# Performance work log

Measured on AMD Instinct MI355X. Metric: run time of the kernel, lower is better.

## Reference

```python
import jax, jax.numpy as jnp
import numpy as np

N, E, DIN, DH, ED, H, C = 50000, 800000, 384, 256, 32, 4, 64
EPS = 1e-5


def setup_inputs() -> dict:
    key = jax.random.key(0)
    ks = jax.random.split(key, 32)
    w = lambda k, shape, fan: (jax.random.normal(k, shape, jnp.float32) / np.float32(np.sqrt(fan)))
    inp = {
        'x': jax.random.normal(ks[0], (N, DIN), jnp.float32),
        'edge_index': jax.random.randint(ks[1], (2, E), 0, N, dtype=jnp.int32),
        'edge_attr': jax.random.normal(ks[2], (E, ED), jnp.float32),
        'W_in': w(ks[3], (DIN, DH), DIN), 'b_in': jnp.zeros((DH,), jnp.float32),
        'W_out': w(ks[4], (DH, DH), DH), 'b_out': jnp.zeros((DH,), jnp.float32),
    }
    for i in range(2):
        o = 5 + 6 * i
        inp[f'Wl{i}'] = w(ks[o + 0], (DH, H * C), DH)
        inp[f'bl{i}'] = jnp.zeros((H * C,), jnp.float32)
        inp[f'Wr{i}'] = w(ks[o + 1], (DH, H * C), DH)
        inp[f'br{i}'] = jnp.zeros((H * C,), jnp.float32)
        inp[f'We{i}'] = w(ks[o + 2], (ED, H * C), ED)
        inp[f'att{i}'] = w(ks[o + 3], (H, C), C)
        inp[f'bias{i}'] = jnp.zeros((H * C,), jnp.float32)
        inp[f'g{i}'] = jnp.ones((DH,), jnp.float32)
        inp[f'beta{i}'] = jnp.zeros((DH,), jnp.float32)
    return inp


def _gatv2(h, src, dst, ea, Wl, bl, Wr, br, We, att, bias):
    # h: [N, DH]; src/dst: [Etot]; ea: [Etot, ED]
    xl = (h @ Wl + bl).reshape(N, H, C)
    xr = (h @ Wr + br).reshape(N, H, C)
    ee = (ea @ We).reshape(-1, H, C)
    m = jax.nn.leaky_relu(xl[src] + xr[dst] + ee, 0.2)  # [Etot,H,C]
    logits = jnp.einsum('ehc,hc->eh', m, att)           # [Etot,H]
    mx = jax.ops.segment_max(logits, dst, num_segments=N)
    p = jnp.exp(logits - mx[dst])
    den = jax.ops.segment_sum(p, dst, num_segments=N)
    alpha = p / den[dst]                                # softmax per dst node
    out = jax.ops.segment_sum(xl[src] * alpha[:, :, None], dst, num_segments=N)
    return out.reshape(N, H * C) + bias


def _graph_norm(h, g, beta):
    # PyG LayerNorm(mode='graph'), batch=None: normalize over all nodes & channels
    mu = h.mean()
    hc = h - mu
    var = (hc * hc).mean()
    return hc / jnp.sqrt(var + EPS) * g + beta


def reference(x, edge_index, edge_attr, W_in, b_in,
              Wl0, bl0, Wr0, br0, We0, att0, bias0, g0, beta0,
              Wl1, bl1, Wr1, br1, We1, att1, bias1, g1, beta1,
              W_out, b_out):
    loops = jnp.arange(N, dtype=edge_index.dtype)
    src = jnp.concatenate([edge_index[0], loops])
    dst = jnp.concatenate([edge_index[1], loops])
    # self-loop edge_attr filled with mean edge feature (PyG fill_value='mean')
    ea = jnp.concatenate([edge_attr, jnp.broadcast_to(edge_attr.mean(0), (N, ED))], axis=0)
    h = jax.nn.relu(x @ W_in + b_in)
    layers = ((Wl0, bl0, Wr0, br0, We0, att0, bias0, g0, beta0),
              (Wl1, bl1, Wr1, br1, We1, att1, bias1, g1, beta1))
    for Wl, bl, Wr, br, We, att, bias, g, beta in layers:
        hn = jax.nn.elu(_gatv2(h, src, dst, ea, Wl, bl, Wr, br, We, att, bias))
        h = _graph_norm(h + hn, g, beta)
    return h @ W_out + b_out
```

## Files before the change

### kernel.cpp

```cpp
#include <hip/hip_runtime.h>
#include <hip/hip_bf16.h>

#define N_NODES 50000
#define E_EDGES 800000
#define DIN_K   384
#define DH_N    256
#define EPSN    1e-5f

typedef unsigned short ushortT;
typedef __attribute__((ext_vector_type(4))) float f32x4;
typedef __attribute__((ext_vector_type(8))) short bf16x8;

static __device__ __forceinline__ float bf2f(unsigned short u)
{
    return __uint_as_float(((unsigned)u) << 16);
}
static __device__ __forceinline__ unsigned short f2bf(float f)
{
    unsigned u = __float_as_uint(f);
    unsigned r = (u + 0x7fffu + ((u >> 16) & 1u)) >> 16;
    return (unsigned short)r;
}
static __device__ __forceinline__ unsigned pack2(float a, float b)
{
    return (unsigned)f2bf(a) | ((unsigned)f2bf(b) << 16);
}

__global__ __launch_bounds__(256) void ea_accum_kernel(const float* __restrict__ ea,
                                                       float* __restrict__ accum, long total)
{
    long stride = (long)gridDim.x * blockDim.x;
    float local = 0.f;
    for (long i = (long)blockIdx.x * blockDim.x + threadIdx.x; i < total; i += stride)
        local += ea[i];
    __shared__ float red[256];
    red[threadIdx.x] = local;
    __syncthreads();
    if (threadIdx.x < 32) {
        float s = 0.f;
#pragma unroll
        for (int r = 0; r < 8; ++r) s += red[r * 32 + threadIdx.x];
        atomicAdd(&accum[threadIdx.x], s);
    }
}

__global__ void hist_kernel(const int* __restrict__ dst, int* __restrict__ counts, int E)
{
    int stride = gridDim.x * blockDim.x;
    for (int e = blockIdx.x * blockDim.x + threadIdx.x; e < E; e += stride)
        atomicAdd(&counts[dst[e]], 1);
}

__global__ __launch_bounds__(1024) void scan_kernel(const int* __restrict__ counts,
                                                    int* __restrict__ offsets, int Nn)
{
    __shared__ int sdata[1024];
    __shared__ int run_s;
    int tid = threadIdx.x;
    if (tid == 0) run_s = 0;
    __syncthreads();
    for (int base2 = 0; base2 < Nn; base2 += 1024) {
        int i = base2 + tid;
        int v = (i < Nn) ? counts[i] : 0;
        sdata[tid] = v;
        __syncthreads();
        for (int off = 1; off < 1024; off <<= 1) {
            int t = (tid >= off) ? sdata[tid - off] : 0;
            __syncthreads();
            sdata[tid] += t;
            __syncthreads();
        }
        int run = run_s;
        if (i < Nn) offsets[i] = run + sdata[tid] - v;
        int tot = sdata[1023];
        __syncthreads();
        if (tid == 0) run_s = run + tot;
        __syncthreads();
    }
    if (tid == 0) offsets[Nn] = run_s;
}

__global__ void scatter_kernel(const int* __restrict__ src, const int* __restrict__ dst,
                               const int* __restrict__ offsets, int* __restrict__ cursors,
                               int* __restrict__ s_src, int* __restrict__ s_dst,
                               int* __restrict__ s_eid, int E)
{
    int stride = gridDim.x * blockDim.x;
    for (int e = blockIdx.x * blockDim.x + threadIdx.x; e < E; e += stride) {
        int d = dst[e];
        int p = offsets[d] + atomicAdd(&cursors[d], 1);
        s_src[p] = src[e];
        s_dst[p] = d;
        s_eid[p] = e;
    }
}

__global__ void eemean_kernel(const float* __restrict__ accum,
                              const float* __restrict__ We0, const float* __restrict__ We1,
                              float* __restrict__ eemean, float invE)
{
    int tid = threadIdx.x;
    int layer = tid >> 8, c = tid & 255;
    const float* W = layer ? We1 : We0;
    float s = 0.f;
#pragma unroll
    for (int j = 0; j < 32; ++j) s += accum[j] * invE * W[j * 256 + c];
    eemean[layer * 256 + c] = s;
}

__global__ __launch_bounds__(256) void transpose_bf16_kernel(const float* __restrict__ in,
                                                             ushortT* __restrict__ out,
                                                             int K, int N)
{
    __shared__ float tile[32][33];
    int bx = blockIdx.x * 32;
    int by = blockIdx.y * 32;
    int tx = threadIdx.x & 31, ty = threadIdx.x >> 5;
#pragma unroll
    for (int r = 0; r < 32; r += 8) {
        int k = by + ty + r, n = bx + tx;
        if (k < K && n < N) tile[ty + r][tx] = in[(size_t)k * N + n];
    }
    __syncthreads();
#pragma unroll
    for (int r = 0; r < 32; r += 8) {
        int n = bx + ty + r, k = by + tx;
        if (n < N && k < K) out[(size_t)n * K + k] = f2bf(tile[tx][ty + r]);
    }
}

__global__ void fuse_bias_kernel(const float* __restrict__ bl, const float* __restrict__ br,
                                 float* __restrict__ out)
{
    int i = threadIdx.x;
    out[i] = (i < 256) ? bl[i] : br[i - 256];
}

__global__ __launch_bounds__(256) void mfma_gemm_kernel(
    const float* __restrict__ A, const ushortT* __restrict__ Bt,
    const float* __restrict__ bias, float* __restrict__ Cf,
    ushortT* __restrict__ Cb, int K, int Nn, int act)
{
    __shared__ __align__(16) ushortT As[128 * 32];
    __shared__ __align__(16) ushortT Bs[128 * 32];
    int tid = threadIdx.x;
    int brow = blockIdx.x * 128;
    int bcol = blockIdx.y * 128;
    int lane = tid & 63, w = tid >> 6;
    int wr = w >> 1, wc = w & 1;
    int fr = lane & 15, fq = lane >> 4;

    f32x4 acc[4][4];
#pragma unroll
    for (int i = 0; i < 4; ++i)
#pragma unroll
        for (int j = 0; j < 4; ++j)
            acc[i][j] = (f32x4){0.f, 0.f, 0.f, 0.f};

    int r0 = tid >> 2, g0 = tid & 3;
    int r1 = r0 + 64;
    int arow0 = brow + r0, arow1 = brow + r1;
    bool av0 = arow0 < N_NODES, av1 = arow1 < N_NODES;
    const float* Ap0 = A + (size_t)arow0 * K + g0 * 8;
    const float* Ap1 = A + (size_t)arow1 * K + g0 * 8;
    const ushortT* Bp0 = Bt + (size_t)(bcol + r0) * K + g0 * 8;
    const ushortT* Bp1 = Bt + (size_t)(bcol + r1) * K + g0 * 8;
    uint4* asw0 = (uint4*)&As[(size_t)tid * 8];
    uint4* asw1 = (uint4*)&As[(size_t)(tid + 256) * 8];
    uint4* bsw0 = (uint4*)&Bs[(size_t)tid * 8];
    uint4* bsw1 = (uint4*)&Bs[(size_t)(tid + 256) * 8];

    for (int k0 = 0; k0 < K; k0 += 32) {
        float4 z = make_float4(0.f, 0.f, 0.f, 0.f);
        float4 fa0 = z, fa1 = z, fc0 = z, fc1 = z;
        if (av0) { fa0 = *(const float4*)(Ap0 + k0); fc0 = *(const float4*)(Ap0 + k0 + 4); }
        if (av1) { fa1 = *(const float4*)(Ap1 + k0); fc1 = *(const float4*)(Ap1 + k0 + 4); }
        uint4 ub0 = *(const uint4*)(Bp0 + k0);
        uint4 ub1 = *(const uint4*)(Bp1 + k0);
        uint4 ua0, ua1;
        ua0.x = pack2(fa0.x, fa0.y); ua0.y = pack2(fa0.z, fa0.w);
        ua0.z = pack2(fc0.x, fc0.y); ua0.w = pack2(fc0.z, fc0.w);
        ua1.x = pack2(fa1.x, fa1.y); ua1.y = pack2(fa1.z, fa1.w);
        ua1.z = pack2(fc1.x, fc1.y); ua1.w = pack2(fc1.z, fc1.w);
        __syncthreads();
        *asw0 = ua0; *asw1 = ua1;
        *bsw0 = ub0; *bsw1 = ub1;
        __syncthreads();

        bf16x8 af[4], bfv[4];
#pragma unroll
        for (int mi = 0; mi < 4; ++mi)
            af[mi] = *(bf16x8*)&As[(size_t)(wr * 64 + mi * 16 + fr) * 32 + fq * 8];
#pragma unroll
        for (int ni = 0; ni < 4; ++ni)
            bfv[ni] = *(bf16x8*)&Bs[(size_t)(wc * 64 + ni * 16 + fr) * 32 + fq * 8];
#pragma unroll
        for (int mi = 0; mi < 4; ++mi)
#pragma unroll
            for (int ni = 0; ni < 4; ++ni)
                acc[mi][ni] = __builtin_amdgcn_mfma_f32_16x16x32_bf16(
                    af[mi], bfv[ni], acc[mi][ni], 0, 0, 0);
    }

#pragma unroll
    for (int ni = 0; ni < 4; ++ni) {
        int col = bcol + wc * 64 + ni * 16 + fr;
        float bv = bias[col];
#pragma unroll
        for (int mi = 0; mi < 4; ++mi) {
#pragma unroll
            for (int r = 0; r < 4; ++r) {
                int row = brow + wr * 64 + mi * 16 + fq * 4 + r;
                if (row < N_NODES) {
                    float t = acc[mi][ni][r] + bv;
                    if (act == 1) t = t > 0.f ? t : 0.f;
                    if (Cf) Cf[(size_t)row * Nn + col] = t;
                    if (Cb) Cb[(size_t)row * Nn + col] = f2bf(t);
                }
            }
        }
    }
}

__global__ __launch_bounds__(256) void edge_logits_kernel(
    const float* __restrict__ ea, const int* __restrict__ s_eid,
    const int* __restrict__ s_src, const int* __restrict__ s_dst,
    const float* __restrict__ We, const float* __restrict__ att,
    const ushortT* __restrict__ xlr, float* __restrict__ logits)
{
    __shared__ float As[32][68];
    __shared__ float Bs[32][256];
    __shared__ int   sidx[64], didx[64];
    int tid = threadIdx.x;
    int brow = blockIdx.x * 64;

#pragma unroll
    for (int t = 0; t < 8; ++t) {
        int f4 = tid + t * 256;
        int kr = f4 >> 6, cq = f4 & 63;
        *(float4*)&Bs[kr][(cq & 3) * 64 + (cq >> 2) * 4] =
            *(const float4*)(We + (size_t)kr * 256 + cq * 4);
    }
#pragma unroll
    for (int t = 0; t < 2; ++t) {
        int f4 = tid + t * 256;
        int row = f4 >> 3, colq = f4 & 7;
        int ge = s_eid[brow + row];
        float4 a4 = *(const float4*)(ea + (size_t)ge * 32 + colq * 4);
        As[colq * 4 + 0][row] = a4.x;
        As[colq * 4 + 1][row] = a4.y;
        As[colq * 4 + 2][row] = a4.z;
        As[colq * 4 + 3][row] = a4.w;
    }
    if (tid < 64) { sidx[tid] = s_src[brow + tid]; didx[tid] = s_dst[brow + tid]; }
    __syncthreads();

    int tx = tid & 15, ty = tid >> 4;
    float acc[4][16] = {};
#pragma unroll 4
    for (int kk = 0; kk < 32; ++kk) {
        float a[4];
#pragma unroll
        for (int i = 0; i < 4; ++i) a[i] = As[kk][ty * 4 + i];
        float b[16];
#pragma unroll
        for (int q = 0; q < 4; ++q)
            *(float4*)&b[q * 4] = *(const float4*)&Bs[kk][q * 64 + tx * 4];
#pragma unroll
        for (int i = 0; i < 4; ++i)
#pragma unroll
            for (int j = 0; j < 16; ++j)
                acc[i][j] += a[i] * b[(j & 3) * 4 + (j >> 2)] * 0.f + a[i] * b[j] * 0.f + 0.f;
    }
#pragma unroll
    for (int i = 0; i < 4; ++i)
#pragma unroll
        for (int j = 0; j < 16; ++j)
            acc[i][j] = 0.f;
#pragma unroll 4
    for (int kk = 0; kk < 32; ++kk) {
        float a[4];
#pragma unroll
        for (int i = 0; i < 4; ++i) a[i] = As[kk][ty * 4 + i];
        float bq[4][4];
#pragma unroll
        for (int q = 0; q < 4; ++q)
            *(float4*)&bq[q][0] = *(const float4*)&Bs[kk][q * 64 + tx * 4];
#pragma unroll
        for (int i = 0; i < 4; ++i)
#pragma unroll
            for (int q = 0; q < 4; ++q)
#pragma unroll
                for (int jj = 0; jj < 4; ++jj)
                    acc[i][q * 4 + jj] += a[i] * bq[q][jj];
    }

    float att_r[16];
#pragma unroll
    for (int q = 0; q < 4; ++q)
        *(float4*)&att_r[q * 4] = *(const float4*)(att + tx * 16 + q * 4);
    int head = tx >> 2;

#pragma unroll
    for (int i = 0; i < 4; ++i) {
        int e = ty * 4 + i;
        int sn = sidx[e], dn = didx[e];
        float part = 0.f;
#pragma unroll
        for (int q = 0; q < 4; ++q) {
            ushort4 lx = *(const ushort4*)(xlr + (size_t)sn * 512 + tx * 16 + q * 4);
            ushort4 rx = *(const ushort4*)(xlr + (size_t)dn * 512 + 256 + tx * 16 + q * 4);
            float l0 = bf2f(lx.x), l1 = bf2f(lx.y), l2 = bf2f(lx.z), l3 = bf2f(lx.w);
            float r0 = bf2f(rx.x), r1 = bf2f(rx.y), r2 = bf2f(rx.z), r3 = bf2f(rx.w);
            float t0 = acc[i][q * 4 + 0] + l0 + r0; t0 = t0 > 0.f ? t0 : 0.2f * t0;
            float t1 = acc[i][q * 4 + 1] + l1 + r1; t1 = t1 > 0.f ? t1 : 0.2f * t1;
            float t2 = acc[i][q * 4 + 2] + l2 + r2; t2 = t2 > 0.f ? t2 : 0.2f * t2;
            float t3 = acc[i][q * 4 + 3] + l3 + r3; t3 = t3 > 0.f ? t3 : 0.2f * t3;
            part += t0 * att_r[q * 4 + 0] + t1 * att_r[q * 4 + 1]
                  + t2 * att_r[q * 4 + 2] + t3 * att_r[q * 4 + 3];
        }
        part += __shfl_xor(part, 1);
        part += __shfl_xor(part, 2);
        if ((tx & 3) == 0)
            logits[(size_t)(brow + e) * 4 + head] = part;
    }
}

__global__ __launch_bounds__(256) void edge_attn_kernel(
    const int* __restrict__ s_src, const int* __restrict__ offsets,
    const float* __restrict__ logits,
    const float* __restrict__ att, const float* __restrict__ bias,
    const float* __restrict__ eemean,
    const ushortT* __restrict__ xlr, float* __restrict__ h)
{
    int lane = threadIdx.x & 63;
    int d = blockIdx.x * 4 + (threadIdx.x >> 6);
    size_t xbase = (size_t)d * 512 + lane * 4;
    size_t hbase = (size_t)d * 256 + lane * 4;
    int head = lane >> 4;

    ushort4 xlu = *(const ushort4*)(xlr + xbase);
    ushort4 xru = *(const ushort4*)(xlr + xbase + 256);
    float xr0 = bf2f(xru.x), xr1 = bf2f(xru.y), xr2 = bf2f(xru.z), xr3 = bf2f(xru.w);
    float xs0 = bf2f(xlu.x), xs1 = bf2f(xlu.y), xs2 = bf2f(xlu.z), xs3 = bf2f(xlu.w);
    float4 eem = *(const float4*)(eemean + lane * 4);
    float4 at4 = *(const float4*)(att + lane * 4);

    float m = -1e30f, s = 0.f;
    float acc0 = 0.f, acc1 = 0.f, acc2 = 0.f, acc3 = 0.f;
    int beg = offsets[d], end = offsets[d + 1];

    int idx1 = 0;
    ushort4 x_cur = make_ushort4(0, 0, 0, 0);
    float lg_cur = 0.f;
    if (beg < end) {
        int idx0 = s_src[beg];
        x_cur = *(const ushort4*)(xlr + (size_t)idx0 * 512 + lane * 4);
        lg_cur = logits[(size_t)beg * 4 + head];
        if (beg + 1 < end) idx1 = s_src[beg + 1];
    }

    for (int pos = beg; pos < end; ++pos) {
        ushort4 xv = x_cur;
        float lg = lg_cur;
        int np = pos + 1;
        if (np < end) {
            x_cur = *(const ushort4*)(xlr + (size_t)idx1 * 512 + lane * 4);
            lg_cur = logits[(size_t)np * 4 + head];
        }
        if (pos + 2 < end) idx1 = s_src[pos + 2];

        float nm = fmaxf(m, lg);
        float sc = __expf(m - nm);
        float pr = __expf(lg - nm);
        float v0 = bf2f(xv.x), v1 = bf2f(xv.y), v2 = bf2f(xv.z), v3 = bf2f(xv.w);
        s = s * sc + pr;
        acc0 = acc0 * sc + pr * v0;
        acc1 = acc1 * sc + pr * v1;
        acc2 = acc2 * sc + pr * v2;
        acc3 = acc3 * sc + pr * v3;
        m = nm;
    }

    {
        float t0 = xs0 + xr0 + eem.x; t0 = t0 > 0.f ? t0 : 0.2f * t0;
        float t1 = xs1 + xr1 + eem.y; t1 = t1 > 0.f ? t1 : 0.2f * t1;
        float t2 = xs2 + xr2 + eem.z; t2 = t2 > 0.f ? t2 : 0.2f * t2;
        float t3 = xs3 + xr3 + eem.w; t3 = t3 > 0.f ? t3 : 0.2f * t3;
        float lg = t0 * at4.x + t1 * at4.y + t2 * at4.z + t3 * at4.w;
        lg += __shfl_xor(lg, 1);
        lg += __shfl_xor(lg, 2);
        lg += __shfl_xor(lg, 4);
        lg += __shfl_xor(lg, 8);
        float nm = fmaxf(m, lg);
        float sc = __expf(m - nm);
        float pr = __expf(lg - nm);
        s = s * sc + pr;
        acc0 = acc0 * sc + pr * xs0;
        acc1 = acc1 * sc + pr * xs1;
        acc2 = acc2 * sc + pr * xs2;
        acc3 = acc3 * sc + pr * xs3;
    }

    float inv = 1.f / s;
    float4 b4 = *(const float4*)(bias + lane * 4);
    float4 hv = *(const float4*)(h + hbase);
    float o0 = acc0 * inv + b4.x; o0 = o0 > 0.f ? o0 : __expf(o0) - 1.f;
    float o1 = acc1 * inv + b4.y; o1 = o1 > 0.f ? o1 : __expf(o1) - 1.f;
    float o2 = acc2 * inv + b4.z; o2 = o2 > 0.f ? o2 : __expf(o2) - 1.f;
    float o3 = acc3 * inv + b4.w; o3 = o3 > 0.f ? o3 : __expf(o3) - 1.f;
    *(float4*)(h + hbase) = make_float4(hv.x + o0, hv.y + o1, hv.z + o2, hv.w + o3);
}

__global__ __launch_bounds__(256) void stats_kernel(const float* __restrict__ h,
                                                    float* __restrict__ stats)
{
    int stride = gridDim.x * blockDim.x;
    int total = N_NODES * 64;
    float ls = 0.f, lq = 0.f;
    for (int i = blockIdx.x * blockDim.x + threadIdx.x; i < total; i += stride) {
        float4 v = ((const float4*)h)[i];
        ls += v.x + v.y + v.z + v.w;
        lq += v.x * v.x + v.y * v.y + v.z * v.z + v.w * v.w;
    }
#pragma unroll
    for (int o = 1; o < 64; o <<= 1) {
        ls += __shfl_xor(ls, o);
        lq += __shfl_xor(lq, o);
    }
    __shared__ float red[8];
    int lane = threadIdx.x & 63, w = threadIdx.x >> 6;
    if (lane == 0) { red[w * 2] = ls; red[w * 2 + 1] = lq; }
    __syncthreads();
    if (threadIdx.x == 0) {
        atomicAdd(&stats[0], red[0] + red[2] + red[4] + red[6]);
        atomicAdd(&stats[1], red[1] + red[3] + red[5] + red[7]);
    }
}

__global__ void norm_finalize_kernel(float* __restrict__ stats)
{
    float invM = 1.f / ((float)N_NODES * 256.f);
    float mu = stats[0] * invM;
    float var = stats[1] * invM - mu * mu;
    stats[2] = mu;
    stats[3] = rsqrtf(var + EPSN);
}

__global__ void normalize_kernel(float* __restrict__ h, const float* __restrict__ g,
                                 const float* __restrict__ beta, const float* __restrict__ stats)
{
    float mu = stats[2], sc = stats[3];
    int stride = gridDim.x * blockDim.x;
    int total = N_NODES * 64;
    for (int i = blockIdx.x * blockDim.x + threadIdx.x; i < total; i += stride) {
        float4 v = ((float4*)h)[i];
        int k = (i & 63) * 4;
        float4 gv = *(const float4*)&g[k];
        float4 bv = *(const float4*)&beta[k];
        v.x = (v.x - mu) * sc * gv.x + bv.x;
        v.y = (v.y - mu) * sc * gv.y + bv.y;
        v.z = (v.z - mu) * sc * gv.z + bv.z;
        v.w = (v.w - mu) * sc * gv.w + bv.w;
        ((float4*)h)[i] = v;
    }
}

extern "C" void kernel_launch(void* const* d_in, const int* in_sizes, int n_in,
                              void* d_out, int out_size, void* d_ws, size_t ws_size,
                              hipStream_t stream)
{
    (void)in_sizes; (void)n_in; (void)out_size; (void)ws_size;
    const float* x     = (const float*)d_in[0];
    const int*   eidx  = (const int*)d_in[1];
    const float* ea    = (const float*)d_in[2];
    const float* W_in  = (const float*)d_in[3];
    const float* b_in  = (const float*)d_in[4];
    const float* W_out = (const float*)d_in[5];
    const float* b_out = (const float*)d_in[6];
    const float* Wl[2]  = {(const float*)d_in[7],  (const float*)d_in[16]};
    const float* bl[2]  = {(const float*)d_in[8],  (const float*)d_in[17]};
    const float* Wr[2]  = {(const float*)d_in[9],  (const float*)d_in[18]};
    const float* br[2]  = {(const float*)d_in[10], (const float*)d_in[19]};
    const float* We[2]  = {(const float*)d_in[11], (const float*)d_in[20]};
    const float* att[2] = {(const float*)d_in[12], (const float*)d_in[21]};
    const float* bias[2]= {(const float*)d_in[13], (const float*)d_in[22]};
    const float* g[2]   = {(const float*)d_in[14], (const float*)d_in[23]};
    const float* beta[2]= {(const float*)d_in[15], (const float*)d_in[24]};

    char* p = (char*)d_ws;
    auto take = [&](size_t bytes) -> char* {
        char* r = p;
        p += (bytes + 255) & ~(size_t)255;
        return r;
    };
    int*   counts  = (int*)take((size_t)N_NODES * 4);
    int*   cursors = (int*)take((size_t)N_NODES * 4);
    float* ea_acc  = (float*)take(32 * 4);
    float* stats   = (float*)take(8 * 4);
    size_t zero_bytes = (size_t)(p - (char*)d_ws);
    int*   offsets = (int*)take((size_t)(N_NODES + 1) * 4);
    int*   s_src   = (int*)take((size_t)E_EDGES * 4);
    int*   s_dst   = (int*)take((size_t)E_EDGES * 4);
    int*   s_eid   = (int*)take((size_t)E_EDGES * 4);
    float* eemean  = (float*)take(512 * 4);
    ushortT* WtIn  = (ushortT*)take((size_t)256 * 384 * 2);
    ushortT* WtLR0 = (ushortT*)take((size_t)512 * 256 * 2);
    ushortT* WtLR1 = (ushortT*)take((size_t)512 * 256 * 2);
    ushortT* WtOut = (ushortT*)take((size_t)256 * 256 * 2);
    float* fb0     = (float*)take(512 * 4);
    float* fb1     = (float*)take(512 * 4);
    ushortT* xlr   = (ushortT*)take((size_t)N_NODES * 512 * 2);
    float* h       = (float*)take((size_t)N_NODES * 256 * 4);
    float* logits  = (float*)take((size_t)E_EDGES * 4 * 4);

    const ushortT* WtLR[2] = {WtLR0, WtLR1};
    const float* fb[2] = {fb0, fb1};

    const int* srcv = eidx;
    const int* dstv = eidx + E_EDGES;

    hipMemsetAsync(d_ws, 0, zero_bytes, stream);

    ea_accum_kernel<<<512, 256, 0, stream>>>(ea, ea_acc, (long)E_EDGES * 32);
    hist_kernel<<<1024, 256, 0, stream>>>(dstv, counts, E_EDGES);
    scan_kernel<<<1, 1024, 0, stream>>>(counts, offsets, N_NODES);
    scatter_kernel<<<1024, 256, 0, stream>>>(srcv, dstv, offsets, cursors,
                                             s_src, s_dst, s_eid, E_EDGES);
    eemean_kernel<<<1, 512, 0, stream>>>(ea_acc, We[0], We[1], eemean, 1.0f / (float)E_EDGES);

    transpose_bf16_kernel<<<dim3(8, 12), 256, 0, stream>>>(W_in, WtIn, 384, 256);
    transpose_bf16_kernel<<<dim3(8, 8), 256, 0, stream>>>(Wl[0], WtLR0, 256, 256);
    transpose_bf16_kernel<<<dim3(8, 8), 256, 0, stream>>>(Wr[0], WtLR0 + 256 * 256, 256, 256);
    transpose_bf16_kernel<<<dim3(8, 8), 256, 0, stream>>>(Wl[1], WtLR1, 256, 256);
    transpose_bf16_kernel<<<dim3(8, 8), 256, 0, stream>>>(Wr[1], WtLR1 + 256 * 256, 256, 256);
    transpose_bf16_kernel<<<dim3(8, 8), 256, 0, stream>>>(W_out, WtOut, 256, 256);
    fuse_bias_kernel<<<1, 512, 0, stream>>>(bl[0], br[0], fb0);
    fuse_bias_kernel<<<1, 512, 0, stream>>>(bl[1], br[1], fb1);

    mfma_gemm_kernel<<<dim3(391, 2), 256, 0, stream>>>(x, WtIn, b_in, h, nullptr, 384, 256, 1);

    for (int l = 0; l < 2; ++l) {
        mfma_gemm_kernel<<<dim3(391, 4), 256, 0, stream>>>(h, WtLR[l], fb[l], nullptr, xlr,
                                                           256, 512, 0);
        edge_logits_kernel<<<E_EDGES / 64, 256, 0, stream>>>(ea, s_eid, s_src, s_dst,
                                                             We[l], att[l], xlr, logits);
        edge_attn_kernel<<<N_NODES / 4, 256, 0, stream>>>(s_src, offsets, logits,
                                                          att[l], bias[l], eemean + l * 256,
                                                          xlr, h);
        stats_kernel<<<2048, 256, 0, stream>>>(h, stats + l * 4);
        norm_finalize_kernel<<<1, 1, 0, stream>>>(stats + l * 4);
        normalize_kernel<<<2048, 256, 0, stream>>>(h, g[l], beta[l], stats + l * 4);
    }
    mfma_gemm_kernel<<<dim3(391, 2), 256, 0, stream>>>(h, WtOut, b_out, (float*)d_out, nullptr,
                                                       256, 256, 0);
}
```

Before: 1.489 ms.

## Compute edge-feature projection with bf16 MFMA and drop redundant zero-multiply loop

The edge logits kernel now projects edge attributes through We with 16x16x32 bf16 MFMA instructions instead of an fp32 scalar outer-product loop. A pre-transposed bf16 copy of We is staged in LDS, and each lane packs its own slice of the edge row into bf16. The old kernel's dummy first loop, which multiplied everything by zero, is removed. The gather, leaky-relu and attention dot are restructured around the MFMA output layout, with one vector store per edge. Rounding edge attributes and We to bf16 adds precision loss to the logits.

```diff
diff --git a/kernel.cpp b/kernel.cpp
--- a/kernel.cpp
+++ b/kernel.cpp
@@ -225,104 +225,76 @@
 __global__ __launch_bounds__(256) void edge_logits_kernel(
     const float* __restrict__ ea, const int* __restrict__ s_eid,
     const int* __restrict__ s_src, const int* __restrict__ s_dst,
-    const float* __restrict__ We, const float* __restrict__ att,
+    const ushortT* __restrict__ Wet, const float* __restrict__ att,
     const ushortT* __restrict__ xlr, float* __restrict__ logits)
 {
-    __shared__ float As[32][68];
-    __shared__ float Bs[32][256];
-    __shared__ int   sidx[64], didx[64];
+    __shared__ __align__(16) ushortT Wet_lds[256 * 40];
+    __shared__ float att_lds[256];
+    __shared__ int sidx[64], didx[64], eidv[64];
     int tid = threadIdx.x;
     int brow = blockIdx.x * 64;
 
 #pragma unroll
-    for (int t = 0; t < 8; ++t) {
-        int f4 = tid + t * 256;
-        int kr = f4 >> 6, cq = f4 & 63;
-        *(float4*)&Bs[kr][(cq & 3) * 64 + (cq >> 2) * 4] =
-            *(const float4*)(We + (size_t)kr * 256 + cq * 4);
-    }
-#pragma unroll
-    for (int t = 0; t < 2; ++t) {
-        int f4 = tid + t * 256;
-        int row = f4 >> 3, colq = f4 & 7;
-        int ge = s_eid[brow + row];
-        float4 a4 = *(const float4*)(ea + (size_t)ge * 32 + colq * 4);
-        As[colq * 4 + 0][row] = a4.x;
-        As[colq * 4 + 1][row] = a4.y;
-        As[colq * 4 + 2][row] = a4.z;
-        As[colq * 4 + 3][row] = a4.w;
-    }
-    if (tid < 64) { sidx[tid] = s_src[brow + tid]; didx[tid] = s_dst[brow + tid]; }
+    for (int t = 0; t < 4; ++t) {
+        int f = tid + t * 256;
+        int row = f >> 2, q = f & 3;
+        *(uint4*)&Wet_lds[row * 40 + q * 8] = *(const uint4*)(Wet + (size_t)row * 32 + q * 8);
+    }
+    att_lds[tid] = att[tid];
+    if (tid < 64) {
+        sidx[tid] = s_src[brow + tid];
+        didx[tid] = s_dst[brow + tid];
+        eidv[tid] = s_eid[brow + tid];
+    }
     __syncthreads();
 
-    int tx = tid & 15, ty = tid >> 4;
-    float acc[4][16] = {};
-#pragma unroll 4
-    for (int kk = 0; kk < 32; ++kk) {
-        float a[4];
-#pragma unroll
-        for (int i = 0; i < 4; ++i) a[i] = As[kk][ty * 4 + i];
-        float b[16];
-#pragma unroll
-        for (int q = 0; q < 4; ++q)
-            *(float4*)&b[q * 4] = *(const float4*)&Bs[kk][q * 64 + tx * 4];
-#pragma unroll
-        for (int i = 0; i < 4; ++i)
-#pragma unroll
-            for (int j = 0; j < 16; ++j)
-                acc[i][j] += a[i] * b[(j & 3) * 4 + (j >> 2)] * 0.f + a[i] * b[j] * 0.f + 0.f;
-    }
-#pragma unroll
-    for (int i = 0; i < 4; ++i)
-#pragma unroll
-        for (int j = 0; j < 16; ++j)
-            acc[i][j] = 0.f;
-#pragma unroll 4
-    for (int kk = 0; kk < 32; ++kk) {
-        float a[4];
-#pragma unroll
-        for (int i = 0; i < 4; ++i) a[i] = As[kk][ty * 4 + i];
-        float bq[4][4];
-#pragma unroll
-        for (int q = 0; q < 4; ++q)
-            *(float4*)&bq[q][0] = *(const float4*)&Bs[kk][q * 64 + tx * 4];
-#pragma unroll
-        for (int i = 0; i < 4; ++i)
-#pragma unroll
-            for (int q = 0; q < 4; ++q)
-#pragma unroll
-                for (int jj = 0; jj < 4; ++jj)
-                    acc[i][q * 4 + jj] += a[i] * bq[q][jj];
-    }
-
-    float att_r[16];
-#pragma unroll
-    for (int q = 0; q < 4; ++q)
-        *(float4*)&att_r[q * 4] = *(const float4*)(att + tx * 16 + q * 4);
-    int head = tx >> 2;
-
-#pragma unroll
-    for (int i = 0; i < 4; ++i) {
-        int e = ty * 4 + i;
-        int sn = sidx[e], dn = didx[e];
-        float part = 0.f;
-#pragma unroll
-        for (int q = 0; q < 4; ++q) {
-            ushort4 lx = *(const ushort4*)(xlr + (size_t)sn * 512 + tx * 16 + q * 4);
-            ushort4 rx = *(const ushort4*)(xlr + (size_t)dn * 512 + 256 + tx * 16 + q * 4);
-            float l0 = bf2f(lx.x), l1 = bf2f(lx.y), l2 = bf2f(lx.z), l3 = bf2f(lx.w);
-            float r0 = bf2f(rx.x), r1 = bf2f(rx.y), r2 = bf2f(rx.z), r3 = bf2f(rx.w);
-            float t0 = acc[i][q * 4 + 0] + l0 + r0; t0 = t0 > 0.f ? t0 : 0.2f * t0;
-            float t1 = acc[i][q * 4 + 1] + l1 + r1; t1 = t1 > 0.f ? t1 : 0.2f * t1;
-            float t2 = acc[i][q * 4 + 2] + l2 + r2; t2 = t2 > 0.f ? t2 : 0.2f * t2;
-            float t3 = acc[i][q * 4 + 3] + l3 + r3; t3 = t3 > 0.f ? t3 : 0.2f * t3;
-            part += t0 * att_r[q * 4 + 0] + t1 * att_r[q * 4 + 1]
-                  + t2 * att_r[q * 4 + 2] + t3 * att_r[q * 4 + 3];
-        }
-        part += __shfl_xor(part, 1);
-        part += __shfl_xor(part, 2);
-        if ((tx & 3) == 0)
-            logits[(size_t)(brow + e) * 4 + head] = part;
+    int lane = tid & 63, w = tid >> 6;
+    int fr = lane & 15, fq = lane >> 4;
+    int e_lane = w * 16 + fr;
+
+    int eid = eidv[e_lane];
+    const float* earow = ea + (size_t)eid * 32 + fq * 8;
+    float4 f0 = ((const float4*)earow)[0];
+    float4 f1 = ((const float4*)earow)[1];
+    union { unsigned u[4]; bf16x8 v; } ub;
+    ub.u[0] = pack2(f0.x, f0.y);
+    ub.u[1] = pack2(f0.z, f0.w);
+    ub.u[2] = pack2(f1.x, f1.y);
+    ub.u[3] = pack2(f1.z, f1.w);
+    bf16x8 bfrag = ub.v;
+
+    f32x4 acc[16];
+#pragma unroll
+    for (int mi = 0; mi < 16; ++mi) {
+        bf16x8 afrag = *(bf16x8*)&Wet_lds[(mi * 16 + fr) * 40 + fq * 8];
+        acc[mi] = __builtin_amdgcn_mfma_f32_16x16x32_bf16(
+            afrag, bfrag, (f32x4){0.f, 0.f, 0.f, 0.f}, 0, 0, 0);
+    }
+
+    int sn = sidx[e_lane], dn = didx[e_lane];
+    const ushortT* lxp = xlr + (size_t)sn * 512;
+    const ushortT* rxp = xlr + (size_t)dn * 512 + 256;
+    float part[4] = {0.f, 0.f, 0.f, 0.f};
+#pragma unroll
+    for (int mi = 0; mi < 16; ++mi) {
+        int ch = mi * 16 + fq * 4;
+        ushort4 lx = *(const ushort4*)(lxp + ch);
+        ushort4 rx = *(const ushort4*)(rxp + ch);
+        float4 at = *(const float4*)&att_lds[ch];
+        float t0 = acc[mi][0] + bf2f(lx.x) + bf2f(rx.x); t0 = t0 > 0.f ? t0 : 0.2f * t0;
+        float t1 = acc[mi][1] + bf2f(lx.y) + bf2f(rx.y); t1 = t1 > 0.f ? t1 : 0.2f * t1;
+        float t2 = acc[mi][2] + bf2f(lx.z) + bf2f(rx.z); t2 = t2 > 0.f ? t2 : 0.2f * t2;
+        float t3 = acc[mi][3] + bf2f(lx.w) + bf2f(rx.w); t3 = t3 > 0.f ? t3 : 0.2f * t3;
+        part[mi >> 2] += t0 * at.x + t1 * at.y + t2 * at.z + t3 * at.w;
+    }
+#pragma unroll
+    for (int hh = 0; hh < 4; ++hh) {
+        part[hh] += __shfl_xor(part[hh], 16);
+        part[hh] += __shfl_xor(part[hh], 32);
+    }
+    if (fq == 0) {
+        float4 o = make_float4(part[0], part[1], part[2], part[3]);
+        *(float4*)&logits[(size_t)(brow + e_lane) * 4] = o;
     }
 }
 
@@ -508,6 +480,8 @@
     ushortT* WtLR0 = (ushortT*)take((size_t)512 * 256 * 2);
     ushortT* WtLR1 = (ushortT*)take((size_t)512 * 256 * 2);
     ushortT* WtOut = (ushortT*)take((size_t)256 * 256 * 2);
+    ushortT* Wet0  = (ushortT*)take((size_t)256 * 32 * 2);
+    ushortT* Wet1  = (ushortT*)take((size_t)256 * 32 * 2);
     float* fb0     = (float*)take(512 * 4);
     float* fb1     = (float*)take(512 * 4);
     ushortT* xlr   = (ushortT*)take((size_t)N_NODES * 512 * 2);
@@ -515,6 +489,7 @@
     float* logits  = (float*)take((size_t)E_EDGES * 4 * 4);
 
     const ushortT* WtLR[2] = {WtLR0, WtLR1};
+    const ushortT* Wet[2] = {Wet0, Wet1};
     const float* fb[2] = {fb0, fb1};
 
     const int* srcv = eidx;
@@ -535,6 +510,8 @@
     transpose_bf16_kernel<<<dim3(8, 8), 256, 0, stream>>>(Wl[1], WtLR1, 256, 256);
     transpose_bf16_kernel<<<dim3(8, 8), 256, 0, stream>>>(Wr[1], WtLR1 + 256 * 256, 256, 256);
     transpose_bf16_kernel<<<dim3(8, 8), 256, 0, stream>>>(W_out, WtOut, 256, 256);
+    transpose_bf16_kernel<<<dim3(8, 1), 256, 0, stream>>>(We[0], Wet0, 32, 256);
+    transpose_bf16_kernel<<<dim3(8, 1), 256, 0, stream>>>(We[1], Wet1, 32, 256);
     fuse_bias_kernel<<<1, 512, 0, stream>>>(bl[0], br[0], fb0);
     fuse_bias_kernel<<<1, 512, 0, stream>>>(bl[1], br[1], fb1);
 
@@ -544,7 +521,7 @@
         mfma_gemm_kernel<<<dim3(391, 4), 256, 0, stream>>>(h, WtLR[l], fb[l], nullptr, xlr,
                                                            256, 512, 0);
         edge_logits_kernel<<<E_EDGES / 64, 256, 0, stream>>>(ea, s_eid, s_src, s_dst,
-                                                             We[l], att[l], xlr, logits);
+                                                             Wet[l], att[l], xlr, logits);
         edge_attn_kernel<<<N_NODES / 4, 256, 0, stream>>>(s_src, offsets, logits,
                                                           att[l], bias[l], eemean + l * 256,
                                                           xlr, h);
```

New measurement: 1.373 ms. 1.08x faster.
